# Performance work log

Hardware: AMD Instinct MI355X
Metric: run time of the kernel (lower is better)

Reference implementation:

```python
import jax, jax.numpy as jnp
import numpy as np

B, T, D, H = 128, 2048, 512, 8
HD = D // H  # head_dim = 64

def setup_inputs() -> dict:
    key = jax.random.key(0)
    ks = jax.random.split(key, 8)
    x = jax.random.normal(ks[0], (B, T, D), dtype=jnp.float32)
    mask_bool = jax.random.randint(ks[1], (B, T), 0, 2) > 0
    temp = jnp.ones((H,), dtype=jnp.float32)
    w_sal = jax.random.normal(ks[2], (D, H), dtype=jnp.float32) * (1.0 / np.sqrt(D))
    b_sal = jnp.zeros((H,), dtype=jnp.float32)
    w_gate = jax.random.normal(ks[3], (HD, 1), dtype=jnp.float32) * (1.0 / np.sqrt(HD))
    b_gate = jnp.zeros((1,), dtype=jnp.float32)
    scale = jnp.ones((D,), dtype=jnp.float32)
    return {"x": x, "mask_bool": mask_bool, "temp": temp, "w_sal": w_sal,
            "b_sal": b_sal, "w_gate": w_gate, "b_gate": b_gate, "scale": scale}

def reference(x, mask_bool, temp, w_sal, b_sal, w_gate, b_gate, scale):
    Bx, Tx, Dx = x.shape
    x_heads = x.reshape(Bx, Tx, H, HD)
    temperature = jax.nn.softplus(temp) + 0.3              # [H]
    logits = (jnp.einsum('btd,dh->bth', x, w_sal) + b_sal) / temperature[None, None, :]
    m = mask_bool[:, :, None]                              # [B,T,1]
    safe_logits = jnp.where(m, logits, -1e9)
    max_logits = jax.lax.stop_gradient(jnp.max(safe_logits, axis=1, keepdims=True))
    exps = jnp.where(m, jnp.exp(safe_logits - max_logits), 0.0)
    weights = exps / (jnp.sum(exps, axis=1, keepdims=True) + 1e-6)  # [B,T,H]
    write_vec_heads = jnp.einsum('bth,bthd->bhd', weights, x_heads)  # [B,H,HD]
    gate_logits = jnp.einsum('bhd,do->bho', write_vec_heads, w_gate) + b_gate  # [B,H,1]
    window_valid = jnp.any(mask_bool, axis=1)[:, None, None]
    write_u_heads = jax.nn.sigmoid(gate_logits) * window_valid.astype(jnp.float32)  # [B,H,1]
    write_vec = write_vec_heads.reshape(Bx, Dx)
    rms = jnp.sqrt(jnp.mean(jnp.square(write_vec), axis=-1, keepdims=True) + 1e-6)
    write_vec = write_vec / rms * scale
    write_u_expanded = jnp.tile(write_u_heads, (1, 1, HD)).reshape(Bx, Dx)
    return (write_vec, write_u_expanded, write_u_heads.squeeze(-1))
```

## Files before the change

kernel.cpp:

```cpp
#include <hip/hip_runtime.h>

#define B_DIM 128
#define T_DIM 2048
#define D_DIM 512
#define H_DIM 8
#define HD_DIM 64
#define CH 8
#define ROWS_PER_BLOCK (T_DIM / CH)
#define ROWS_PER_WAVE (ROWS_PER_BLOCK / 4)
#define SUBS (CH * 4)

typedef float f4v __attribute__((ext_vector_type(4)));

__global__ void detect_mask_kernel(const int* __restrict__ mask_as_int,
                                   int* __restrict__ flag) {
    const unsigned v = (unsigned)mask_as_int[threadIdx.x];
    const unsigned long long bb = __ballot(v > 1u);
    if (threadIdx.x == 0) *flag = (bb != 0ull) ? 1 : 0;
}

#define ROW_BODY(ROW, B0, B1)                                                  \
  {                                                                            \
    const int row_ = (ROW);                                                    \
               \
    float p0 = B0.x * w[0];                                                    \
    float p1 = B0.x * w[1];                                                    \
    float p2 = B0.x * w[2];                                                    \
    float p3 = B0.x * w[3];                                                    \
    float p4 = B0.x * w[4];                                                    \
    float p5 = B0.x * w[5];                                                    \
    float p6 = B0.x * w[6];                                                    \
    float p7 = B0.x * w[7];                                                    \
    p0 = fmaf(B0.y, w[8+0], p0);  p1 = fmaf(B0.y, w[8+1], p1);                 \
    p2 = fmaf(B0.y, w[8+2], p2);  p3 = fmaf(B0.y, w[8+3], p3);                 \
    p4 = fmaf(B0.y, w[8+4], p4);  p5 = fmaf(B0.y, w[8+5], p5);                 \
    p6 = fmaf(B0.y, w[8+6], p6);  p7 = fmaf(B0.y, w[8+7], p7);                 \
    p0 = fmaf(B0.z, w[16+0], p0); p1 = fmaf(B0.z, w[16+1], p1);                \
    p2 = fmaf(B0.z, w[16+2], p2); p3 = fmaf(B0.z, w[16+3], p3);                \
    p4 = fmaf(B0.z, w[16+4], p4); p5 = fmaf(B0.z, w[16+5], p5);                \
    p6 = fmaf(B0.z, w[16+6], p6); p7 = fmaf(B0.z, w[16+7], p7);                \
    p0 = fmaf(B0.w, w[24+0], p0); p1 = fmaf(B0.w, w[24+1], p1);                \
    p2 = fmaf(B0.w, w[24+2], p2); p3 = fmaf(B0.w, w[24+3], p3);                \
    p4 = fmaf(B0.w, w[24+4], p4); p5 = fmaf(B0.w, w[24+5], p5);                \
    p6 = fmaf(B0.w, w[24+6], p6); p7 = fmaf(B0.w, w[24+7], p7);                \
    p0 = fmaf(B1.x, w[32+0], p0); p1 = fmaf(B1.x, w[32+1], p1);                \
    p2 = fmaf(B1.x, w[32+2], p2); p3 = fmaf(B1.x, w[32+3], p3);                \
    p4 = fmaf(B1.x, w[32+4], p4); p5 = fmaf(B1.x, w[32+5], p5);                \
    p6 = fmaf(B1.x, w[32+6], p6); p7 = fmaf(B1.x, w[32+7], p7);                \
    p0 = fmaf(B1.y, w[40+0], p0); p1 = fmaf(B1.y, w[40+1], p1);                \
    p2 = fmaf(B1.y, w[40+2], p2); p3 = fmaf(B1.y, w[40+3], p3);                \
    p4 = fmaf(B1.y, w[40+4], p4); p5 = fmaf(B1.y, w[40+5], p5);                \
    p6 = fmaf(B1.y, w[40+6], p6); p7 = fmaf(B1.y, w[40+7], p7);                \
    p0 = fmaf(B1.z, w[48+0], p0); p1 = fmaf(B1.z, w[48+1], p1);                \
    p2 = fmaf(B1.z, w[48+2], p2); p3 = fmaf(B1.z, w[48+3], p3);                \
    p4 = fmaf(B1.z, w[48+4], p4); p5 = fmaf(B1.z, w[48+5], p5);                \
    p6 = fmaf(B1.z, w[48+6], p6); p7 = fmaf(B1.z, w[48+7], p7);                \
    p0 = fmaf(B1.w, w[56+0], p0); p1 = fmaf(B1.w, w[56+1], p1);                \
    p2 = fmaf(B1.w, w[56+2], p2); p3 = fmaf(B1.w, w[56+3], p3);                \
    p4 = fmaf(B1.w, w[56+4], p4); p5 = fmaf(B1.w, w[56+5], p5);                \
    p6 = fmaf(B1.w, w[56+6], p6); p7 = fmaf(B1.w, w[56+7], p7);                \
                              \
    const bool hi5 = (lane & 32) != 0;                                         \
    float q0 = (hi5 ? p4 : p0) + __shfl_xor(hi5 ? p0 : p4, 32, 64);            \
    float q1 = (hi5 ? p5 : p1) + __shfl_xor(hi5 ? p1 : p5, 32, 64);            \
    float q2 = (hi5 ? p6 : p2) + __shfl_xor(hi5 ? p2 : p6, 32, 64);            \
    float q3 = (hi5 ? p7 : p3) + __shfl_xor(hi5 ? p3 : p7, 32, 64);            \
    const bool hi4 = (lane & 16) != 0;                                         \
    float r0 = (hi4 ? q2 : q0) + __shfl_xor(hi4 ? q0 : q2, 16, 64);            \
    float r1 = (hi4 ? q3 : q1) + __shfl_xor(hi4 ? q1 : q3, 16, 64);            \
    const bool hi3 = (lane & 8) != 0;                                          \
    float s = (hi3 ? r1 : r0) + __shfl_xor(hi3 ? r0 : r1, 8, 64);              \
    s += __shfl_xor(s, 4, 64);                                                 \
    s += __shfl_xor(s, 2, 64);                                                 \
    s += __shfl_xor(s, 1, 64);                                                 \
    const bool valid = (rowmask >> row_) & 1ull;                               \
    const float lg  = (s + bs) * invT;                                         \
    const float lgv = valid ? lg : -1e9f;                                      \
    const bool need = lgv > m + 8.0f;                                          \
    if (__any(need)) {                                                         \
      const float mn = need ? lgv : m;                                         \
      const float sc = __expf(m - mn);                                         \
      l *= sc;                                                                 \
      acc0 *= sc; acc1 *= sc; acc2 *= sc; acc3 *= sc;                          \
      acc4 *= sc; acc5 *= sc; acc6 *= sc; acc7 *= sc;                          \
      m = mn;                                                                  \
    }                                                                          \
    const float pe = valid ? __expf(lgv - m) : 0.0f;                           \
    l += pe;                                                                   \
    acc0 = fmaf(pe, B0.x, acc0); acc1 = fmaf(pe, B0.y, acc1);                  \
    acc2 = fmaf(pe, B0.z, acc2); acc3 = fmaf(pe, B0.w, acc3);                  \
    acc4 = fmaf(pe, B1.x, acc4); acc5 = fmaf(pe, B1.y, acc5);                  \
    acc6 = fmaf(pe, B1.z, acc6); acc7 = fmaf(pe, B1.w, acc7);                  \
           \
    const int pr_ = (row_ + 2 < ROWS_PER_WAVE) ? (row_ + 2)                    \
                                               : (ROWS_PER_WAVE - 1);          \
    const f4v* pp_ = xbase + (size_t)pr_ * (D_DIM / 4);                        \
    B0 = pp_[0];                                                               \
    B1 = pp_[1];                                                               \
  }

__global__ __launch_bounds__(256, 4) void salience_pass1(
    const float* __restrict__ x,
    const void* __restrict__ mask,
    const float* __restrict__ temp,
    const float* __restrict__ w_sal,
    const float* __restrict__ b_sal,
    const int* __restrict__ flag,
    float* __restrict__ ws_m,
    float* __restrict__ ws_l,
    float* __restrict__ ws_acc)
{
    const int b     = blockIdx.x >> 3;
    const int chunk = blockIdx.x & 7;
    const int lane  = threadIdx.x & 63;
    const int wv    = threadIdx.x >> 6;
    const int h     = lane >> 3;

    const int byte_mask = *flag;

    float w[64];
    {
        const float4* wp = (const float4*)w_sal + (size_t)lane * 16;
        #pragma unroll
        for (int q = 0; q < 16; ++q) {
            float4 v = wp[q];
            w[q*4+0] = v.x; w[q*4+1] = v.y; w[q*4+2] = v.z; w[q*4+3] = v.w;
        }
    }
    const float bs = b_sal[h];
    const float tp = temp[h];
    const float sp = (tp > 20.0f) ? tp : log1pf(__expf(tp));
    const float invT = 1.0f / (sp + 0.3f);

    const int t0 = chunk * ROWS_PER_BLOCK + wv * ROWS_PER_WAVE;
    const size_t mbase = (size_t)b * T_DIM + t0;

    int mv = byte_mask ? (int)((const unsigned char*)mask)[mbase + lane]
                       : ((const int*)mask)[mbase + lane];
    const unsigned long long rowmask = __ballot(mv != 0);

    float m = -1e9f;
    float l = 0.0f;
    float acc0 = 0.f, acc1 = 0.f, acc2 = 0.f, acc3 = 0.f;
    float acc4 = 0.f, acc5 = 0.f, acc6 = 0.f, acc7 = 0.f;

    const f4v* xbase = (const f4v*)(x + ((size_t)b * T_DIM + t0) * D_DIM)
                       + (size_t)lane * 2;

    f4v bA0 = xbase[0];
    f4v bA1 = xbase[1];
    f4v bB0 = xbase[D_DIM / 4];
    f4v bB1 = xbase[D_DIM / 4 + 1];

    for (int r2 = 0; r2 < ROWS_PER_WAVE / 2; ++r2) {
        ROW_BODY(2 * r2,     bA0, bA1)
        ROW_BODY(2 * r2 + 1, bB0, bB1)
    }

    const int sub = chunk * 4 + wv;
    const size_t bc = (size_t)b * SUBS + sub;
    if ((lane & 7) == 0) {
        ws_m[bc * H_DIM + h] = m;
        ws_l[bc * H_DIM + h] = l;
    }
    float4* dst = (float4*)(ws_acc + bc * D_DIM + (size_t)lane * 8);
    dst[0] = make_float4(acc0, acc1, acc2, acc3);
    dst[1] = make_float4(acc4, acc5, acc6, acc7);
}

__global__ __launch_bounds__(512) void salience_pass2(
    const float* __restrict__ ws_m,
    const float* __restrict__ ws_l,
    const float* __restrict__ ws_acc,
    const float* __restrict__ w_gate,
    const float* __restrict__ b_gate,
    const float* __restrict__ scale,
    float* __restrict__ out)
{
    const int b  = blockIdx.x;
    const int d  = threadIdx.x;
    const int h  = d >> 6;
    const int dd = d & 63;
    const int lane = d & 63;

    __shared__ float sm_e[SUBS * H_DIM];
    __shared__ float sm_L[H_DIM];
    __shared__ float red[H_DIM];

    {
        const int c = lane & 31;
        const size_t idx = ((size_t)b * SUBS + c) * H_DIM + h;
        const float mv = ws_m[idx];
        const float lv = ws_l[idx];
        float M = mv;
        M = fmaxf(M, __shfl_xor(M, 16, 64));
        M = fmaxf(M, __shfl_xor(M, 8, 64));
        M = fmaxf(M, __shfl_xor(M, 4, 64));
        M = fmaxf(M, __shfl_xor(M, 2, 64));
        M = fmaxf(M, __shfl_xor(M, 1, 64));
        const float e = __expf(mv - M);
        float Lp = lv * e;
        Lp += __shfl_xor(Lp, 16, 64);
        Lp += __shfl_xor(Lp, 8, 64);
        Lp += __shfl_xor(Lp, 4, 64);
        Lp += __shfl_xor(Lp, 2, 64);
        Lp += __shfl_xor(Lp, 1, 64);
        if (lane < 32) sm_e[c * H_DIM + h] = e;
        if (lane == 0) sm_L[h] = Lp;
    }
    __syncthreads();

    float A = 0.0f;
    const float* pa = ws_acc + (size_t)b * SUBS * D_DIM + d;
    #pragma unroll
    for (int c0 = 0; c0 < SUBS; c0 += 8) {
        float v0 = pa[(size_t)(c0+0) * D_DIM];
        float v1 = pa[(size_t)(c0+1) * D_DIM];
        float v2 = pa[(size_t)(c0+2) * D_DIM];
        float v3 = pa[(size_t)(c0+3) * D_DIM];
        float v4 = pa[(size_t)(c0+4) * D_DIM];
        float v5 = pa[(size_t)(c0+5) * D_DIM];
        float v6 = pa[(size_t)(c0+6) * D_DIM];
        float v7 = pa[(size_t)(c0+7) * D_DIM];
        A = fmaf(sm_e[(c0+0) * H_DIM + h], v0, A);
        A = fmaf(sm_e[(c0+1) * H_DIM + h], v1, A);
        A = fmaf(sm_e[(c0+2) * H_DIM + h], v2, A);
        A = fmaf(sm_e[(c0+3) * H_DIM + h], v3, A);
        A = fmaf(sm_e[(c0+4) * H_DIM + h], v4, A);
        A = fmaf(sm_e[(c0+5) * H_DIM + h], v5, A);
        A = fmaf(sm_e[(c0+6) * H_DIM + h], v6, A);
        A = fmaf(sm_e[(c0+7) * H_DIM + h], v7, A);
    }
    const float L = sm_L[h];
    const float wv = A / (L + 1e-6f);

    float g = wv * w_gate[dd];
    #pragma unroll
    for (int s = 1; s < 64; s <<= 1) g += __shfl_xor(g, s, 64);
    const float gl = g + b_gate[0];
    const float u = (L > 0.0f) ? (1.0f / (1.0f + __expf(-gl))) : 0.0f;

    float sq = wv * wv;
    #pragma unroll
    for (int s = 1; s < 64; s <<= 1) sq += __shfl_xor(sq, s, 64);
    if (dd == 0) red[h] = sq;
    __syncthreads();
    float ssum = 0.0f;
    #pragma unroll
    for (int k = 0; k < H_DIM; ++k) ssum += red[k];
    const float rms = sqrtf(ssum * (1.0f / (float)D_DIM) + 1e-6f);

    out[(size_t)b * D_DIM + d] = wv / rms * scale[d];
    out[(size_t)B_DIM * D_DIM + (size_t)b * D_DIM + d] = u;
    if (dd == 0) out[2 * (size_t)B_DIM * D_DIM + (size_t)b * H_DIM + h] = u;
}

extern "C" void kernel_launch(void* const* d_in, const int* in_sizes, int n_in,
                              void* d_out, int out_size, void* d_ws, size_t ws_size,
                              hipStream_t stream) {
    (void)in_sizes; (void)n_in; (void)out_size; (void)ws_size;
    const float* x      = (const float*)d_in[0];
    const void*  mask   = d_in[1];
    const float* temp   = (const float*)d_in[2];
    const float* w_sal  = (const float*)d_in[3];
    const float* b_sal  = (const float*)d_in[4];
    const float* w_gate = (const float*)d_in[5];
    const float* b_gate = (const float*)d_in[6];
    const float* scale  = (const float*)d_in[7];
    float* out = (float*)d_out;

    char* ws = (char*)d_ws;
    int*   flag   = (int*)ws;
    float* ws_m   = (float*)(ws + 256);
    float* ws_l   = (float*)(ws + 256 + 131072);
    float* ws_acc = (float*)(ws + 256 + 2 * 131072);

    detect_mask_kernel<<<1, 64, 0, stream>>>((const int*)mask, flag);
    salience_pass1<<<B_DIM * CH, 256, 0, stream>>>(
        x, mask, temp, w_sal, b_sal, flag, ws_m, ws_l, ws_acc);
    salience_pass2<<<B_DIM, 512, 0, stream>>>(
        ws_m, ws_l, ws_acc, w_gate, b_gate, scale, out);
}
```

Baseline: 119.1 us.

## Remap lanes to coalesced float4 columns with two heads per lane; inline mask detection

Each lane now loads one float4 from the first half of the row and one from the second half, so it covers two heads instead of one contiguous 8-float slice. This gives fully coalesced 16-byte accesses across the wave. The shuffle reduction is restructured to produce two head logits per lane, with a separate online-softmax state kept for each head. The separate mask-type detection kernel is removed and its ballot is recomputed inside every block, which saves one launch at the cost of a small redundant load per block.

```diff
diff --git a/kernel.cpp b/kernel.cpp
--- a/kernel.cpp
+++ b/kernel.cpp
@@ -12,17 +12,10 @@
 
 typedef float f4v __attribute__((ext_vector_type(4)));
 
-__global__ void detect_mask_kernel(const int* __restrict__ mask_as_int,
-                                   int* __restrict__ flag) {
-    const unsigned v = (unsigned)mask_as_int[threadIdx.x];
-    const unsigned long long bb = __ballot(v > 1u);
-    if (threadIdx.x == 0) *flag = (bb != 0ull) ? 1 : 0;
-}
-
 #define ROW_BODY(ROW, B0, B1)                                                  \
   {                                                                            \
     const int row_ = (ROW);                                                    \
-               \
+            \
     float p0 = B0.x * w[0];                                                    \
     float p1 = B0.x * w[1];                                                    \
     float p2 = B0.x * w[2];                                                    \
@@ -59,44 +52,47 @@
     p2 = fmaf(B1.w, w[56+2], p2); p3 = fmaf(B1.w, w[56+3], p3);                \
     p4 = fmaf(B1.w, w[56+4], p4); p5 = fmaf(B1.w, w[56+5], p5);                \
     p6 = fmaf(B1.w, w[56+6], p6); p7 = fmaf(B1.w, w[56+7], p7);                \
-                              \
-    const bool hi5 = (lane & 32) != 0;                                         \
-    float q0 = (hi5 ? p4 : p0) + __shfl_xor(hi5 ? p0 : p4, 32, 64);            \
-    float q1 = (hi5 ? p5 : p1) + __shfl_xor(hi5 ? p1 : p5, 32, 64);            \
-    float q2 = (hi5 ? p6 : p2) + __shfl_xor(hi5 ? p2 : p6, 32, 64);            \
-    float q3 = (hi5 ? p7 : p3) + __shfl_xor(hi5 ? p3 : p7, 32, 64);            \
-    const bool hi4 = (lane & 16) != 0;                                         \
-    float r0 = (hi4 ? q2 : q0) + __shfl_xor(hi4 ? q0 : q2, 16, 64);            \
-    float r1 = (hi4 ? q3 : q1) + __shfl_xor(hi4 ? q1 : q3, 16, 64);            \
-    const bool hi3 = (lane & 8) != 0;                                          \
-    float s = (hi3 ? r1 : r0) + __shfl_xor(hi3 ? r0 : r1, 8, 64);              \
-    s += __shfl_xor(s, 4, 64);                                                 \
-    s += __shfl_xor(s, 2, 64);                                                 \
-    s += __shfl_xor(s, 1, 64);                                                 \
+            \
+    const bool hi5 = (lane & 32) != 0;                         \
+    float q0 = (hi5 ? p2 : p0) + __shfl_xor(hi5 ? p0 : p2, 32, 64);            \
+    float q1 = (hi5 ? p3 : p1) + __shfl_xor(hi5 ? p1 : p3, 32, 64);            \
+    float q2 = (hi5 ? p6 : p4) + __shfl_xor(hi5 ? p4 : p6, 32, 64);            \
+    float q3 = (hi5 ? p7 : p5) + __shfl_xor(hi5 ? p5 : p7, 32, 64);            \
+    const bool hi4 = (lane & 16) != 0;                         \
+    float sA = (hi4 ? q1 : q0) + __shfl_xor(hi4 ? q0 : q1, 16, 64);            \
+    float sB = (hi4 ? q3 : q2) + __shfl_xor(hi4 ? q2 : q3, 16, 64);            \
+    sA += __shfl_xor(sA, 8, 64);  sB += __shfl_xor(sB, 8, 64);                 \
+    sA += __shfl_xor(sA, 4, 64);  sB += __shfl_xor(sB, 4, 64);                 \
+    sA += __shfl_xor(sA, 2, 64);  sB += __shfl_xor(sB, 2, 64);                 \
+    sA += __shfl_xor(sA, 1, 64);  sB += __shfl_xor(sB, 1, 64);                 \
     const bool valid = (rowmask >> row_) & 1ull;                               \
-    const float lg  = (s + bs) * invT;                                         \
-    const float lgv = valid ? lg : -1e9f;                                      \
-    const bool need = lgv > m + 8.0f;                                          \
-    if (__any(need)) {                                                         \
-      const float mn = need ? lgv : m;                                         \
-      const float sc = __expf(m - mn);                                         \
-      l *= sc;                                                                 \
-      acc0 *= sc; acc1 *= sc; acc2 *= sc; acc3 *= sc;                          \
-      acc4 *= sc; acc5 *= sc; acc6 *= sc; acc7 *= sc;                          \
-      m = mn;                                                                  \
+    const float lgA = valid ? (sA + bsA) * invTA : -1e9f;                      \
+    const float lgB = valid ? (sB + bsB) * invTB : -1e9f;                      \
+    const bool needA = lgA > mA + 8.0f;                                        \
+    const bool needB = lgB > mB + 8.0f;                                        \
+    if (__any(needA || needB)) {                                               \
+      const float mnA = needA ? lgA : mA;                                      \
+      const float scA = __expf(mA - mnA);                                      \
+      const float mnB = needB ? lgB : mB;                                      \
+      const float scB = __expf(mB - mnB);                                      \
+      lA *= scA; lB *= scB;                                                    \
+      acc0 *= scA; acc1 *= scA; acc2 *= scA; acc3 *= scA;                      \
+      acc4 *= scB; acc5 *= scB; acc6 *= scB; acc7 *= scB;                      \
+      mA = mnA; mB = mnB;                                                      \
     }                                                                          \
-    const float pe = valid ? __expf(lgv - m) : 0.0f;                           \
-    l += pe;                                                                   \
-    acc0 = fmaf(pe, B0.x, acc0); acc1 = fmaf(pe, B0.y, acc1);                  \
-    acc2 = fmaf(pe, B0.z, acc2); acc3 = fmaf(pe, B0.w, acc3);                  \
-    acc4 = fmaf(pe, B1.x, acc4); acc5 = fmaf(pe, B1.y, acc5);                  \
-    acc6 = fmaf(pe, B1.z, acc6); acc7 = fmaf(pe, B1.w, acc7);                  \
+    const float peA = valid ? __expf(lgA - mA) : 0.0f;                         \
+    const float peB = valid ? __expf(lgB - mB) : 0.0f;                         \
+    lA += peA; lB += peB;                                                      \
+    acc0 = fmaf(peA, B0.x, acc0); acc1 = fmaf(peA, B0.y, acc1);                \
+    acc2 = fmaf(peA, B0.z, acc2); acc3 = fmaf(peA, B0.w, acc3);                \
+    acc4 = fmaf(peB, B1.x, acc4); acc5 = fmaf(peB, B1.y, acc5);                \
+    acc6 = fmaf(peB, B1.z, acc6); acc7 = fmaf(peB, B1.w, acc7);                \
            \
     const int pr_ = (row_ + 2 < ROWS_PER_WAVE) ? (row_ + 2)                    \
                                                : (ROWS_PER_WAVE - 1);          \
-    const f4v* pp_ = xbase + (size_t)pr_ * (D_DIM / 4);                        \
+    const f4v* pp_ = xb + (size_t)pr_ * (D_DIM / 4);                           \
     B0 = pp_[0];                                                               \
-    B1 = pp_[1];                                                               \
+    B1 = pp_[64];                                                              \
   }
 
 __global__ __launch_bounds__(256, 4) void salience_pass1(
@@ -105,7 +101,6 @@
     const float* __restrict__ temp,
     const float* __restrict__ w_sal,
     const float* __restrict__ b_sal,
-    const int* __restrict__ flag,
     float* __restrict__ ws_m,
     float* __restrict__ ws_l,
     float* __restrict__ ws_acc)
@@ -114,43 +109,53 @@
     const int chunk = blockIdx.x & 7;
     const int lane  = threadIdx.x & 63;
     const int wv    = threadIdx.x >> 6;
-    const int h     = lane >> 3;
-
-    const int byte_mask = *flag;
+    const int hA    = lane >> 4;
+
+    const unsigned mv0 = (unsigned)((const int*)mask)[lane];
+    const int byte_mask = (__ballot(mv0 > 1u) != 0ull) ? 1 : 0;
 
     float w[64];
     {
-        const float4* wp = (const float4*)w_sal + (size_t)lane * 16;
+        const float4* wa = (const float4*)(w_sal) + (size_t)lane * 8;
+        const float4* wb = (const float4*)(w_sal + 2048) + (size_t)lane * 8;
         #pragma unroll
-        for (int q = 0; q < 16; ++q) {
-            float4 v = wp[q];
+        for (int q = 0; q < 8; ++q) {
+            float4 v = wa[q];
             w[q*4+0] = v.x; w[q*4+1] = v.y; w[q*4+2] = v.z; w[q*4+3] = v.w;
         }
-    }
-    const float bs = b_sal[h];
-    const float tp = temp[h];
-    const float sp = (tp > 20.0f) ? tp : log1pf(__expf(tp));
-    const float invT = 1.0f / (sp + 0.3f);
+        #pragma unroll
+        for (int q = 0; q < 8; ++q) {
+            float4 v = wb[q];
+            w[32+q*4+0] = v.x; w[32+q*4+1] = v.y; w[32+q*4+2] = v.z; w[32+q*4+3] = v.w;
+        }
+    }
+    const float bsA = b_sal[hA];
+    const float bsB = b_sal[hA + 4];
+    const float tpA = temp[hA];
+    const float tpB = temp[hA + 4];
+    const float spA = (tpA > 20.0f) ? tpA : log1pf(__expf(tpA));
+    const float spB = (tpB > 20.0f) ? tpB : log1pf(__expf(tpB));
+    const float invTA = 1.0f / (spA + 0.3f);
+    const float invTB = 1.0f / (spB + 0.3f);
 
     const int t0 = chunk * ROWS_PER_BLOCK + wv * ROWS_PER_WAVE;
     const size_t mbase = (size_t)b * T_DIM + t0;
 
-    int mv = byte_mask ? (int)((const unsigned char*)mask)[mbase + lane]
-                       : ((const int*)mask)[mbase + lane];
-    const unsigned long long rowmask = __ballot(mv != 0);
-
-    float m = -1e9f;
-    float l = 0.0f;
+    int mrow = byte_mask ? (int)((const unsigned char*)mask)[mbase + lane]
+                         : ((const int*)mask)[mbase + lane];
+    const unsigned long long rowmask = __ballot(mrow != 0);
+
+    float mA = -1e9f, lA = 0.0f;
+    float mB = -1e9f, lB = 0.0f;
     float acc0 = 0.f, acc1 = 0.f, acc2 = 0.f, acc3 = 0.f;
     float acc4 = 0.f, acc5 = 0.f, acc6 = 0.f, acc7 = 0.f;
 
-    const f4v* xbase = (const f4v*)(x + ((size_t)b * T_DIM + t0) * D_DIM)
-                       + (size_t)lane * 2;
-
-    f4v bA0 = xbase[0];
-    f4v bA1 = xbase[1];
-    f4v bB0 = xbase[D_DIM / 4];
-    f4v bB1 = xbase[D_DIM / 4 + 1];
+    const f4v* xb = (const f4v*)(x + ((size_t)b * T_DIM + t0) * D_DIM) + lane;
+
+    f4v bA0 = xb[0];
+    f4v bA1 = xb[64];
+    f4v bB0 = xb[128];
+    f4v bB1 = xb[192];
 
     for (int r2 = 0; r2 < ROWS_PER_WAVE / 2; ++r2) {
         ROW_BODY(2 * r2,     bA0, bA1)
@@ -159,13 +164,15 @@
 
     const int sub = chunk * 4 + wv;
     const size_t bc = (size_t)b * SUBS + sub;
-    if ((lane & 7) == 0) {
-        ws_m[bc * H_DIM + h] = m;
-        ws_l[bc * H_DIM + h] = l;
-    }
-    float4* dst = (float4*)(ws_acc + bc * D_DIM + (size_t)lane * 8);
-    dst[0] = make_float4(acc0, acc1, acc2, acc3);
-    dst[1] = make_float4(acc4, acc5, acc6, acc7);
+    if ((lane & 15) == 0) {
+        ws_m[bc * H_DIM + hA]     = mA;
+        ws_m[bc * H_DIM + hA + 4] = mB;
+        ws_l[bc * H_DIM + hA]     = lA;
+        ws_l[bc * H_DIM + hA + 4] = lB;
+    }
+    float4* dstA = (float4*)(ws_acc + bc * D_DIM) + lane;
+    dstA[0]  = make_float4(acc0, acc1, acc2, acc3);
+    dstA[64] = make_float4(acc4, acc5, acc6, acc7);
 }
 
 __global__ __launch_bounds__(512) void salience_pass2(
@@ -270,14 +277,12 @@
     float* out = (float*)d_out;
 
     char* ws = (char*)d_ws;
-    int*   flag   = (int*)ws;
     float* ws_m   = (float*)(ws + 256);
     float* ws_l   = (float*)(ws + 256 + 131072);
     float* ws_acc = (float*)(ws + 256 + 2 * 131072);
 
-    detect_mask_kernel<<<1, 64, 0, stream>>>((const int*)mask, flag);
     salience_pass1<<<B_DIM * CH, 256, 0, stream>>>(
-        x, mask, temp, w_sal, b_sal, flag, ws_m, ws_l, ws_acc);
+        x, mask, temp, w_sal, b_sal, ws_m, ws_l, ws_acc);
     salience_pass2<<<B_DIM, 512, 0, stream>>>(
         ws_m, ws_l, ws_acc, w_gate, b_gate, scale, out);
 }
```

Result: faster. 115.6 us (-2.9%).
